# Performance work log

Hardware: AMD Instinct MI355X
Metric: run time of the kernel (lower is better)

## Reference

```python
import jax, jax.numpy as jnp
import numpy as np

EMB = 768
HEADS = 8

def setup_inputs() -> dict:
    key = jax.random.key(0)
    ks = jax.random.split(key, 9)
    B, N, E = 16, 1024, EMB
    s = 1.0 / np.sqrt(E)
    x = jax.random.normal(ks[0], (B, N, E), dtype=jnp.float32)
    Wq = jax.random.normal(ks[1], (E, E), dtype=jnp.float32) * s
    bq = jnp.zeros((E,), dtype=jnp.float32)
    Wk = jax.random.normal(ks[2], (E, E), dtype=jnp.float32) * s
    bk = jnp.zeros((E,), dtype=jnp.float32)
    Wv = jax.random.normal(ks[3], (E, E), dtype=jnp.float32) * s
    bv = jnp.zeros((E,), dtype=jnp.float32)
    Wo = jax.random.normal(ks[4], (E, E), dtype=jnp.float32) * s
    bo = jnp.zeros((E,), dtype=jnp.float32)
    return {"x": x, "Wq": Wq, "bq": bq, "Wk": Wk, "bk": bk, "Wv": Wv, "bv": bv, "Wo": Wo, "bo": bo}

def reference(x, Wq, bq, Wk, bk, Wv, bv, Wo, bo):
    B, N, E = x.shape
    H = HEADS
    D = E // H
    # separate Q/K/V linears, split heads: b n (h d) -> b h n d
    q = (x @ Wq + bq).reshape(B, N, H, D).transpose(0, 2, 1, 3)
    k = (x @ Wk + bk).reshape(B, N, H, D).transpose(0, 2, 1, 3)
    v = (x @ Wv + bv).reshape(B, N, H, D).transpose(0, 2, 1, 3)
    energy = jnp.einsum('bhqd,bhkd->bhqk', q, k)
    # NON-STANDARD: softmax first, then divide by sqrt(emb_size)
    scaling = jnp.float32(E) ** 0.5
    attn = jax.nn.softmax(energy, axis=-1) / scaling
    out = jnp.einsum('bhqk,bhkd->bhqd', attn, v)
    out = out.transpose(0, 2, 1, 3).reshape(B, N, E)  # b h n d -> b n (h d)
    return out @ Wo + bo
```

## Files before the change

kernel.cpp:

```cpp
#include <hip/hip_runtime.h>


typedef _Float16 half8 __attribute__((ext_vector_type(8)));
typedef __fp16 fp16x2 __attribute__((ext_vector_type(2)));
typedef float f32x4 __attribute__((ext_vector_type(4)));

__device__ __forceinline__ void gload_lds16(const void* g, void* l) {
  __builtin_amdgcn_global_load_lds((const __attribute__((address_space(1))) void*)g,
                                   (__attribute__((address_space(3))) void*)l, 16, 0, 0);
}


__global__ __launch_bounds__(256) void conv_x_kernel(const float* __restrict__ x,
                                                     _Float16* __restrict__ xh) {
  long i = ((long)blockIdx.x * 256 + threadIdx.x) * 8;
  float4 a = *(const float4*)(x + i);
  float4 b = *(const float4*)(x + i + 4);
  half8 o;
  o[0] = (_Float16)a.x; o[1] = (_Float16)a.y; o[2] = (_Float16)a.z; o[3] = (_Float16)a.w;
  o[4] = (_Float16)b.x; o[5] = (_Float16)b.y; o[6] = (_Float16)b.z; o[7] = (_Float16)b.w;
  *(half8*)(xh + i) = o;
}

__global__ __launch_bounds__(256) void transpose_cvt_kernel(
    const float* __restrict__ W0, const float* __restrict__ W1,
    const float* __restrict__ W2, const float* __restrict__ W3,
    _Float16* __restrict__ WT) {
  __shared__ float tile[32][33];
  int z = blockIdx.z;
  const float* W = (z == 0) ? W0 : (z == 1) ? W1 : (z == 2) ? W2 : W3;
  int k0 = blockIdx.y * 32, n0 = blockIdx.x * 32;
  int tx = threadIdx.x, ty = threadIdx.y;
#pragma unroll
  for (int j = ty; j < 32; j += 8)
    tile[j][tx] = W[(size_t)(k0 + j) * 768 + n0 + tx];
  __syncthreads();
  _Float16* dst = WT + (size_t)z * 768 * 768;
#pragma unroll
  for (int j = ty; j < 32; j += 8)
    dst[(size_t)(n0 + j) * 768 + k0 + tx] = (_Float16)tile[tx][j];
}

__global__ __launch_bounds__(256) void conv_bias_kernel(const float* __restrict__ bq,
                                                        const float* __restrict__ bk,
                                                        const float* __restrict__ bv,
                                                        float* __restrict__ bias) {
  int i = blockIdx.x * 256 + threadIdx.x;
  if (i >= 2304) return;
  bias[i] = (i < 768) ? bq[i] : (i < 1536) ? bk[i - 768] : bv[i - 1536];
}


template <int OUT_F16>
__global__ __launch_bounds__(512, 2) void gemm256_kernel(
    const _Float16* __restrict__ A, const _Float16* __restrict__ Bt,
    const float* __restrict__ bias, void* __restrict__ C,
    int M, int N, int K, int ldc) {
  __shared__ _Float16 As[2][256 * 64];
  __shared__ _Float16 Bs[2][256 * 64];
  int nbx = N >> 8;
  int nwg = gridDim.x, wg = blockIdx.x;
  int cpx = nwg >> 3;
  int swz = (wg & 7) * cpx + (wg >> 3);
  int bx = swz % nbx, by = swz / nbx;
  int m0 = by * 256, n0 = bx * 256;
  int t = threadIdx.x, l = t & 63, w = t >> 6;
  int lg = l >> 4, lr = l & 15;
  int wr = w >> 2, wc = w & 3;
  f32x4 acc[8][4] = {};

  int srow[4], ssc[4];
#pragma unroll
  for (int j = 0; j < 4; ++j) {
    int slot = j * 512 + t;
    srow[j] = slot >> 3;
    ssc[j] = ((slot & 7) ^ (srow[j] & 7)) * 8;
  }

  auto stage = [&](int kt, int bi) {
    int k0 = kt * 64;
#pragma unroll
    for (int j = 0; j < 4; ++j)
      gload_lds16(A + (size_t)(m0 + srow[j]) * K + k0 + ssc[j], &As[bi][(j * 512 + t) * 8]);
#pragma unroll
    for (int j = 0; j < 4; ++j)
      gload_lds16(Bt + (size_t)(n0 + srow[j]) * K + k0 + ssc[j], &Bs[bi][(j * 512 + t) * 8]);
  };

  auto compute = [&](int bi) {
#pragma unroll
    for (int kk = 0; kk < 2; ++kk) {
      half8 bf[4];
#pragma unroll
      for (int nf = 0; nf < 4; ++nf) {
        int row = wc * 64 + nf * 16 + lr;
        bf[nf] = *(const half8*)&Bs[bi][row * 64 + ((kk * 4 + lg) ^ (row & 7)) * 8];
      }
#pragma unroll
      for (int mf = 0; mf < 8; ++mf) {
        int row = wr * 128 + mf * 16 + lr;
        half8 af = *(const half8*)&As[bi][row * 64 + ((kk * 4 + lg) ^ (row & 7)) * 8];
#pragma unroll
        for (int nf = 0; nf < 4; ++nf)
          acc[mf][nf] = __builtin_amdgcn_mfma_f32_16x16x32_f16(af, bf[nf], acc[mf][nf], 0, 0, 0);
      }
    }
  };

  int nkt = K >> 6;
  stage(0, 0);
  for (int kt = 0; kt < nkt; ++kt) {
    int bi = kt & 1;
    if (kt + 1 < nkt) {
      stage(kt + 1, bi ^ 1);
      asm volatile("s_waitcnt vmcnt(8)" ::: "memory");
    } else {
      asm volatile("s_waitcnt vmcnt(0)" ::: "memory");
    }
    __builtin_amdgcn_sched_barrier(0);
    __builtin_amdgcn_s_barrier();
    __builtin_amdgcn_sched_barrier(0);
    compute(bi);
    __builtin_amdgcn_sched_barrier(0);
    __builtin_amdgcn_s_barrier();
  }

#pragma unroll
  for (int mf = 0; mf < 8; ++mf)
#pragma unroll
    for (int nf = 0; nf < 4; ++nf) {
      int col = n0 + wc * 64 + nf * 16 + lr;
      float bb = bias[col];
#pragma unroll
      for (int i = 0; i < 4; ++i) {
        int row = m0 + wr * 128 + mf * 16 + lg * 4 + i;
        float v = acc[mf][nf][i] + bb;
        if (OUT_F16)
          ((_Float16*)C)[(size_t)row * ldc + col] = (_Float16)v;
        else
          ((float*)C)[(size_t)row * ldc + col] = v;
      }
    }
}


__global__ __launch_bounds__(512) void attn_kernel(const _Float16* __restrict__ QKV,
                                                   _Float16* __restrict__ Oh) {
  int hw = blockIdx.x;
  int lin = (hw & 7) * 128 + (hw >> 3);
  int bh = lin >> 3, qt = lin & 7;
  int b = bh >> 3, h = bh & 7;
  int t = threadIdx.x, w = t >> 6, l = t & 63;
  int lg = l >> 4, lr = l & 15;

  __shared__ _Float16 Ks[2][64 * 128];
  __shared__ _Float16 Vts[2][96 * 64];
  __shared__ _Float16 Ps[8][16 * 64];

  const _Float16* Qb = QKV + (size_t)b * 1024 * 2304 + h * 96;
  const _Float16* Kb = Qb + 768;
  const _Float16* Vb = Qb + 1536;

  half8 qf[3];
  {
    int qrow = qt * 128 + w * 16 + lr;
    const _Float16 s = (_Float16)1.4426950408889634f;
#pragma unroll
    for (int c = 0; c < 3; ++c) {
      qf[c] = *(const half8*)&Qb[(size_t)qrow * 2304 + c * 32 + lg * 8];
#pragma unroll
      for (int e = 0; e < 8; ++e) qf[c][e] = qf[c][e] * s;
    }
  }

  int ksrc[2], kdst[2];
#pragma unroll
  for (int j = 0; j < 2; ++j) {
    int slot = j * 512 + t;
    int kv = slot >> 4, seg = slot & 15;
    ksrc[j] = kv * 2304 + (seg ^ (kv & 7)) * 8;
    kdst[j] = slot * 8;
  }
  bool vact = t < 384;
  int kvp = t / 12, m = t % 12;
  int vsrc = 2 * kvp * 2304 + m * 8;
  int vdst[8];
#pragma unroll
  for (int e = 0; e < 8; ++e) {
    int d = m * 8 + e;
    int sw = ((d & 7) ^ ((d >> 3) & 7)) << 3;
    vdst[e] = d * 64 + ((2 * kvp) ^ sw);
  }
  int swq = (lr & 7) << 3;
  int poff[4];
#pragma unroll
  for (int tt = 0; tt < 4; ++tt) poff[tt] = lr * 64 + ((tt * 16 + lg * 4) ^ swq);

  auto stage = [&](int kv0, int bi) {
    size_t goff = (size_t)kv0 * 2304;
#pragma unroll
    for (int j = 0; j < 2; ++j)
      gload_lds16(Kb + goff + ksrc[j], &Ks[bi][kdst[j]]);
    if (vact) {
      const _Float16* vp = Vb + goff + vsrc;
      half8 v0 = *(const half8*)vp;
      half8 v1 = *(const half8*)(vp + 2304);
#pragma unroll
      for (int e = 0; e < 8; ++e) {
        union { _Float16 h2[2]; unsigned u32; } pk;
        pk.h2[0] = v0[e]; pk.h2[1] = v1[e];
        *(unsigned*)&Vts[bi][vdst[e]] = pk.u32;
      }
    }
  };

  float m_run = -3.0e38f, l_run = 0.f;
  f32x4 o_acc[6] = {};

  stage(0, 0);

  for (int tile = 0; tile < 16; ++tile) {
    int bi = tile & 1;
    __syncthreads();
    if (tile + 1 < 16) stage((tile + 1) * 64, bi ^ 1);

    f32x4 s_acc[4];
#pragma unroll
    for (int tt = 0; tt < 4; ++tt) {
      s_acc[tt] = f32x4{0.f, 0.f, 0.f, 0.f};
      int kvr = tt * 16 + lr;
#pragma unroll
      for (int c = 0; c < 3; ++c) {
        half8 kf = *(const half8*)&Ks[bi][kvr * 128 + ((c * 4 + lg) ^ (kvr & 7)) * 8];
        s_acc[tt] = __builtin_amdgcn_mfma_f32_16x16x32_f16(kf, qf[c], s_acc[tt], 0, 0, 0);
      }
    }

    float tmax = -3.0e38f;
#pragma unroll
    for (int tt = 0; tt < 4; ++tt)
#pragma unroll
      for (int i = 0; i < 4; ++i) tmax = fmaxf(tmax, s_acc[tt][i]);
    tmax = fmaxf(tmax, __shfl_xor(tmax, 16, 64));
    tmax = fmaxf(tmax, __shfl_xor(tmax, 32, 64));

    if (!__all(tmax <= m_run + 11.5f)) {
      float m_new = fmaxf(m_run, tmax);
      float scale = __builtin_exp2f(m_run - m_new);
      float sc0 = __shfl(scale, lg * 4 + 0, 64);
      float sc1 = __shfl(scale, lg * 4 + 1, 64);
      float sc2 = __shfl(scale, lg * 4 + 2, 64);
      float sc3 = __shfl(scale, lg * 4 + 3, 64);
#pragma unroll
      for (int cc = 0; cc < 6; ++cc) {
        o_acc[cc][0] *= sc0; o_acc[cc][1] *= sc1;
        o_acc[cc][2] *= sc2; o_acc[cc][3] *= sc3;
      }
      l_run *= scale;
      m_run = m_new;
    }

    float rs = 0.f;
#pragma unroll
    for (int tt = 0; tt < 4; ++tt) {
      float p0 = __builtin_exp2f(s_acc[tt][0] - m_run);
      float p1 = __builtin_exp2f(s_acc[tt][1] - m_run);
      float p2 = __builtin_exp2f(s_acc[tt][2] - m_run);
      float p3 = __builtin_exp2f(s_acc[tt][3] - m_run);
      rs += (p0 + p1) + (p2 + p3);
      union { fp16x2 h2[2]; unsigned long long u64; } pk;
      pk.h2[0] = __builtin_amdgcn_cvt_pkrtz(p0, p1);
      pk.h2[1] = __builtin_amdgcn_cvt_pkrtz(p2, p3);
      *(unsigned long long*)&Ps[w][poff[tt]] = pk.u64;
    }
    rs += __shfl_xor(rs, 16, 64);
    rs += __shfl_xor(rs, 32, 64);
    l_run += rs;

#pragma unroll
    for (int kc = 0; kc < 2; ++kc) {
      half8 pf = *(const half8*)&Ps[w][lr * 64 + ((kc * 32 + lg * 8) ^ swq)];
#pragma unroll
      for (int cc = 0; cc < 6; ++cc) {
        int d = cc * 16 + lr;
        int sw = ((d & 7) ^ ((d >> 3) & 7)) << 3;
        half8 vf = *(const half8*)&Vts[bi][d * 64 + ((kc * 32 + lg * 8) ^ sw)];
        o_acc[cc] = __builtin_amdgcn_mfma_f32_16x16x32_f16(pf, vf, o_acc[cc], 0, 0, 0);
      }
    }
  }

  float inv = 1.0f / (l_run * 27.712812921102035f);
  float iv0 = __shfl(inv, lg * 4 + 0, 64);
  float iv1 = __shfl(inv, lg * 4 + 1, 64);
  float iv2 = __shfl(inv, lg * 4 + 2, 64);
  float iv3 = __shfl(inv, lg * 4 + 3, 64);
  size_t rbase = (size_t)(b * 1024 + qt * 128 + w * 16) * 768 + h * 96;
#pragma unroll
  for (int cc = 0; cc < 6; ++cc) {
    int col = cc * 16 + lr;
    Oh[rbase + (size_t)(lg * 4 + 0) * 768 + col] = (_Float16)(o_acc[cc][0] * iv0);
    Oh[rbase + (size_t)(lg * 4 + 1) * 768 + col] = (_Float16)(o_acc[cc][1] * iv1);
    Oh[rbase + (size_t)(lg * 4 + 2) * 768 + col] = (_Float16)(o_acc[cc][2] * iv2);
    Oh[rbase + (size_t)(lg * 4 + 3) * 768 + col] = (_Float16)(o_acc[cc][3] * iv3);
  }
}


extern "C" void kernel_launch(void* const* d_in, const int* in_sizes, int n_in,
                              void* d_out, int out_size, void* d_ws, size_t ws_size,
                              hipStream_t stream) {
  const float* x  = (const float*)d_in[0];
  const float* Wq = (const float*)d_in[1];
  const float* bq = (const float*)d_in[2];
  const float* Wk = (const float*)d_in[3];
  const float* bk = (const float*)d_in[4];
  const float* Wv = (const float*)d_in[5];
  const float* bv = (const float*)d_in[6];
  const float* Wo = (const float*)d_in[7];
  const float* bo = (const float*)d_in[8];
  float* out = (float*)d_out;

  char* ws = (char*)d_ws;
  _Float16* WT   = (_Float16*)(ws);
  float*    bias = (float*)(ws + 4718592);
  _Float16* xh   = (_Float16*)(ws + 4751360);
  _Float16* QKV  = (_Float16*)(ws + 29917184);
  _Float16* Oh   = (_Float16*)(ws + 105414656);

  conv_x_kernel<<<6144, 256, 0, stream>>>(x, xh);
  transpose_cvt_kernel<<<dim3(24, 24, 4), dim3(32, 8), 0, stream>>>(Wq, Wk, Wv, Wo, WT);
  conv_bias_kernel<<<9, 256, 0, stream>>>(bq, bk, bv, bias);

  gemm256_kernel<1><<<576, 512, 0, stream>>>(xh, WT, bias, QKV, 16384, 2304, 768, 2304);

  attn_kernel<<<1024, 512, 0, stream>>>(QKV, Oh);

  gemm256_kernel<0><<<192, 512, 0, stream>>>(Oh, WT + (size_t)2304 * 768, bo, out,
                                             16384, 768, 768, 768);
}
```

Measured before the change: 232.5 us.

## Rewrite attention with 32x32x16 MFMA, register-resident P, 4-wave blocks

The attention kernel moves from 16x16x32 to 32x32x16 MFMA tiles, with each wave owning 32 query rows. K is staged into LDS already in MFMA fragment order. The P matrix no longer round-trips through LDS; lanes swap halves with a cross-lane shuffle to form the A operand for the PV MFMA. Blocks drop to 256 threads with a two-blocks-per-CU launch bound, which cuts LDS traffic and P staging at the cost of more registers per lane and extra shuffles.

Result: slower. 420.6 us (+80.9%).

```diff
diff --git a/kernel.cpp b/kernel.cpp
--- a/kernel.cpp
+++ b/kernel.cpp
@@ -4,6 +4,7 @@
 typedef _Float16 half8 __attribute__((ext_vector_type(8)));
 typedef __fp16 fp16x2 __attribute__((ext_vector_type(2)));
 typedef float f32x4 __attribute__((ext_vector_type(4)));
+typedef float f32x16 __attribute__((ext_vector_type(16)));
 
 __device__ __forceinline__ void gload_lds16(const void* g, void* l) {
   __builtin_amdgcn_global_load_lds((const __attribute__((address_space(1))) void*)g,
@@ -144,78 +145,81 @@
 }
 
 
-__global__ __launch_bounds__(512) void attn_kernel(const _Float16* __restrict__ QKV,
-                                                   _Float16* __restrict__ Oh) {
+__global__ __launch_bounds__(256, 2) void attn_kernel(const _Float16* __restrict__ QKV,
+                                                      _Float16* __restrict__ Oh) {
   int hw = blockIdx.x;
   int lin = (hw & 7) * 128 + (hw >> 3);
   int bh = lin >> 3, qt = lin & 7;
   int b = bh >> 3, h = bh & 7;
   int t = threadIdx.x, w = t >> 6, l = t & 63;
-  int lg = l >> 4, lr = l & 15;
-
-  __shared__ _Float16 Ks[2][64 * 128];
-  __shared__ _Float16 Vts[2][96 * 64];
-  __shared__ _Float16 Ps[8][16 * 64];
+  int lr = l & 31, hi = l >> 5;
+
+  __shared__ __align__(16) char KF[2][12288];
+  __shared__ __align__(16) _Float16 VF[2][96 * 64];
 
   const _Float16* Qb = QKV + (size_t)b * 1024 * 2304 + h * 96;
   const _Float16* Kb = Qb + 768;
   const _Float16* Vb = Qb + 1536;
 
-  half8 qf[3];
+  half8 qf[6];
   {
-    int qrow = qt * 128 + w * 16 + lr;
+    int qrow = qt * 128 + w * 32 + lr;
     const _Float16 s = (_Float16)1.4426950408889634f;
 #pragma unroll
-    for (int c = 0; c < 3; ++c) {
-      qf[c] = *(const half8*)&Qb[(size_t)qrow * 2304 + c * 32 + lg * 8];
+    for (int c = 0; c < 6; ++c) {
+      qf[c] = *(const half8*)&Qb[(size_t)qrow * 2304 + c * 16 + hi * 8];
 #pragma unroll
       for (int e = 0; e < 8; ++e) qf[c][e] = qf[c][e] * s;
     }
   }
 
-  int ksrc[2], kdst[2];
+  int ks_src[3], ks_dst[3];
+#pragma unroll
+  for (int j = 0; j < 3; ++j) {
+    int s = j * 256 + t;
+    int f = s >> 6, lane = s & 63;
+    int sb = f / 6, c = f - sb * 6;
+    ks_src[j] = (sb * 32 + (lane & 31)) * 2304 + c * 16 + ((lane >> 5) & 1) * 8;
+    ks_dst[j] = s * 16;
+  }
+  bool vact[2];
+  int v_src[2], v_dst[2][8];
 #pragma unroll
   for (int j = 0; j < 2; ++j) {
-    int slot = j * 512 + t;
-    int kv = slot >> 4, seg = slot & 15;
-    ksrc[j] = kv * 2304 + (seg ^ (kv & 7)) * 8;
-    kdst[j] = slot * 8;
-  }
-  bool vact = t < 384;
-  int kvp = t / 12, m = t % 12;
-  int vsrc = 2 * kvp * 2304 + m * 8;
-  int vdst[8];
-#pragma unroll
-  for (int e = 0; e < 8; ++e) {
-    int d = m * 8 + e;
-    int sw = ((d & 7) ^ ((d >> 3) & 7)) << 3;
-    vdst[e] = d * 64 + ((2 * kvp) ^ sw);
-  }
-  int swq = (lr & 7) << 3;
-  int poff[4];
-#pragma unroll
-  for (int tt = 0; tt < 4; ++tt) poff[tt] = lr * 64 + ((tt * 16 + lg * 4) ^ swq);
+    int u = j * 256 + t;
+    vact[j] = u < 384;
+    int kvp = u / 12, mm = u % 12;
+    v_src[j] = 2 * kvp * 2304 + mm * 8;
+#pragma unroll
+    for (int e = 0; e < 8; ++e) {
+      int d = mm * 8 + e;
+      int sw = ((d & 7) ^ ((d >> 3) & 7)) << 3;
+      v_dst[j][e] = d * 64 + ((2 * kvp) ^ sw);
+    }
+  }
 
   auto stage = [&](int kv0, int bi) {
     size_t goff = (size_t)kv0 * 2304;
 #pragma unroll
+    for (int j = 0; j < 3; ++j)
+      gload_lds16(Kb + goff + ks_src[j], &KF[bi][ks_dst[j]]);
+#pragma unroll
     for (int j = 0; j < 2; ++j)
-      gload_lds16(Kb + goff + ksrc[j], &Ks[bi][kdst[j]]);
-    if (vact) {
-      const _Float16* vp = Vb + goff + vsrc;
-      half8 v0 = *(const half8*)vp;
-      half8 v1 = *(const half8*)(vp + 2304);
-#pragma unroll
-      for (int e = 0; e < 8; ++e) {
-        union { _Float16 h2[2]; unsigned u32; } pk;
-        pk.h2[0] = v0[e]; pk.h2[1] = v1[e];
-        *(unsigned*)&Vts[bi][vdst[e]] = pk.u32;
-      }
-    }
+      if (vact[j]) {
+        const _Float16* vp = Vb + goff + v_src[j];
+        half8 v0 = *(const half8*)vp;
+        half8 v1 = *(const half8*)(vp + 2304);
+#pragma unroll
+        for (int e = 0; e < 8; ++e) {
+          union { _Float16 h2[2]; unsigned u32; } pk;
+          pk.h2[0] = v0[e]; pk.h2[1] = v1[e];
+          *(unsigned*)&VF[bi][v_dst[j][e]] = pk.u32;
+        }
+      }
   };
 
   float m_run = -3.0e38f, l_run = 0.f;
-  f32x4 o_acc[6] = {};
+  f32x16 oa[3] = {};
 
   stage(0, 0);
 
@@ -224,85 +228,89 @@
     __syncthreads();
     if (tile + 1 < 16) stage((tile + 1) * 64, bi ^ 1);
 
-    f32x4 s_acc[4];
-#pragma unroll
-    for (int tt = 0; tt < 4; ++tt) {
-      s_acc[tt] = f32x4{0.f, 0.f, 0.f, 0.f};
-      int kvr = tt * 16 + lr;
-#pragma unroll
-      for (int c = 0; c < 3; ++c) {
-        half8 kf = *(const half8*)&Ks[bi][kvr * 128 + ((c * 4 + lg) ^ (kvr & 7)) * 8];
-        s_acc[tt] = __builtin_amdgcn_mfma_f32_16x16x32_f16(kf, qf[c], s_acc[tt], 0, 0, 0);
-      }
-    }
+    f32x16 sA[2] = {};
+#pragma unroll
+    for (int sb = 0; sb < 2; ++sb)
+#pragma unroll
+      for (int c = 0; c < 6; ++c) {
+        half8 kf = *(const half8*)(KF[bi] + (sb * 6 + c) * 1024 + l * 16);
+        sA[sb] = __builtin_amdgcn_mfma_f32_32x32x16_f16(kf, qf[c], sA[sb], 0, 0, 0);
+      }
 
     float tmax = -3.0e38f;
 #pragma unroll
-    for (int tt = 0; tt < 4; ++tt)
-#pragma unroll
-      for (int i = 0; i < 4; ++i) tmax = fmaxf(tmax, s_acc[tt][i]);
-    tmax = fmaxf(tmax, __shfl_xor(tmax, 16, 64));
+    for (int sb = 0; sb < 2; ++sb)
+#pragma unroll
+      for (int r = 0; r < 16; ++r) tmax = fmaxf(tmax, sA[sb][r]);
     tmax = fmaxf(tmax, __shfl_xor(tmax, 32, 64));
 
     if (!__all(tmax <= m_run + 11.5f)) {
       float m_new = fmaxf(m_run, tmax);
       float scale = __builtin_exp2f(m_run - m_new);
-      float sc0 = __shfl(scale, lg * 4 + 0, 64);
-      float sc1 = __shfl(scale, lg * 4 + 1, 64);
-      float sc2 = __shfl(scale, lg * 4 + 2, 64);
-      float sc3 = __shfl(scale, lg * 4 + 3, 64);
-#pragma unroll
-      for (int cc = 0; cc < 6; ++cc) {
-        o_acc[cc][0] *= sc0; o_acc[cc][1] *= sc1;
-        o_acc[cc][2] *= sc2; o_acc[cc][3] *= sc3;
+#pragma unroll
+      for (int r = 0; r < 16; ++r) {
+        float sr = __shfl(scale, (r & 3) + 8 * (r >> 2) + 4 * hi, 64);
+        oa[0][r] *= sr; oa[1][r] *= sr; oa[2][r] *= sr;
       }
       l_run *= scale;
       m_run = m_new;
     }
 
+    unsigned keep[8], send[8];
     float rs = 0.f;
 #pragma unroll
-    for (int tt = 0; tt < 4; ++tt) {
-      float p0 = __builtin_exp2f(s_acc[tt][0] - m_run);
-      float p1 = __builtin_exp2f(s_acc[tt][1] - m_run);
-      float p2 = __builtin_exp2f(s_acc[tt][2] - m_run);
-      float p3 = __builtin_exp2f(s_acc[tt][3] - m_run);
-      rs += (p0 + p1) + (p2 + p3);
-      union { fp16x2 h2[2]; unsigned long long u64; } pk;
-      pk.h2[0] = __builtin_amdgcn_cvt_pkrtz(p0, p1);
-      pk.h2[1] = __builtin_amdgcn_cvt_pkrtz(p2, p3);
-      *(unsigned long long*)&Ps[w][poff[tt]] = pk.u64;
-    }
-    rs += __shfl_xor(rs, 16, 64);
+    for (int sb = 0; sb < 2; ++sb)
+#pragma unroll
+      for (int kb = 0; kb < 2; ++kb)
+#pragma unroll
+        for (int m = 0; m < 2; ++m) {
+          int rk = 2 * m + 8 * kb + 4 * hi;
+          int rq = 2 * m + 8 * kb + 4 * (1 - hi);
+          float k0 = __builtin_exp2f(sA[sb][rk] - m_run);
+          float k1 = __builtin_exp2f(sA[sb][rk + 1] - m_run);
+          float q0 = __builtin_exp2f(sA[sb][rq] - m_run);
+          float q1 = __builtin_exp2f(sA[sb][rq + 1] - m_run);
+          rs += (k0 + k1) + (q0 + q1);
+          union { fp16x2 h2; unsigned u; } a, bb;
+          a.h2 = __builtin_amdgcn_cvt_pkrtz(k0, k1);
+          bb.h2 = __builtin_amdgcn_cvt_pkrtz(q0, q1);
+          keep[sb * 4 + kb * 2 + m] = a.u;
+          send[sb * 4 + kb * 2 + m] = bb.u;
+        }
     rs += __shfl_xor(rs, 32, 64);
     l_run += rs;
 
-#pragma unroll
-    for (int kc = 0; kc < 2; ++kc) {
-      half8 pf = *(const half8*)&Ps[w][lr * 64 + ((kc * 32 + lg * 8) ^ swq)];
-#pragma unroll
-      for (int cc = 0; cc < 6; ++cc) {
-        int d = cc * 16 + lr;
+    unsigned recv[8];
+#pragma unroll
+    for (int i = 0; i < 8; ++i) recv[i] = __shfl_xor(send[i], 32, 64);
+
+#pragma unroll
+    for (int kstep = 0; kstep < 4; ++kstep) {
+      int base = (kstep >> 1) * 4 + (kstep & 1) * 2;
+      union { unsigned u[4]; half8 h8; } pa;
+      pa.u[0] = hi ? recv[base + 0] : keep[base + 0];
+      pa.u[1] = hi ? recv[base + 1] : keep[base + 1];
+      pa.u[2] = hi ? keep[base + 0] : recv[base + 0];
+      pa.u[3] = hi ? keep[base + 1] : recv[base + 1];
+#pragma unroll
+      for (int dt = 0; dt < 3; ++dt) {
+        int d = dt * 32 + lr;
         int sw = ((d & 7) ^ ((d >> 3) & 7)) << 3;
-        half8 vf = *(const half8*)&Vts[bi][d * 64 + ((kc * 32 + lg * 8) ^ sw)];
-        o_acc[cc] = __builtin_amdgcn_mfma_f32_16x16x32_f16(pf, vf, o_acc[cc], 0, 0, 0);
+        half8 vf = *(const half8*)&VF[bi][d * 64 + ((kstep * 16 + hi * 8) ^ sw)];
+        oa[dt] = __builtin_amdgcn_mfma_f32_32x32x16_f16(pa.h8, vf, oa[dt], 0, 0, 0);
       }
     }
   }
 
   float inv = 1.0f / (l_run * 27.712812921102035f);
-  float iv0 = __shfl(inv, lg * 4 + 0, 64);
-  float iv1 = __shfl(inv, lg * 4 + 1, 64);
-  float iv2 = __shfl(inv, lg * 4 + 2, 64);
-  float iv3 = __shfl(inv, lg * 4 + 3, 64);
-  size_t rbase = (size_t)(b * 1024 + qt * 128 + w * 16) * 768 + h * 96;
-#pragma unroll
-  for (int cc = 0; cc < 6; ++cc) {
-    int col = cc * 16 + lr;
-    Oh[rbase + (size_t)(lg * 4 + 0) * 768 + col] = (_Float16)(o_acc[cc][0] * iv0);
-    Oh[rbase + (size_t)(lg * 4 + 1) * 768 + col] = (_Float16)(o_acc[cc][1] * iv1);
-    Oh[rbase + (size_t)(lg * 4 + 2) * 768 + col] = (_Float16)(o_acc[cc][2] * iv2);
-    Oh[rbase + (size_t)(lg * 4 + 3) * 768 + col] = (_Float16)(o_acc[cc][3] * iv3);
+  size_t rbase = (size_t)(b * 1024 + qt * 128 + w * 32) * 768 + h * 96;
+#pragma unroll
+  for (int r = 0; r < 16; ++r) {
+    int q = (r & 3) + 8 * (r >> 2) + 4 * hi;
+    float ivr = __shfl(inv, q, 64);
+#pragma unroll
+    for (int dt = 0; dt < 3; ++dt)
+      Oh[rbase + (size_t)q * 768 + dt * 32 + lr] = (_Float16)(oa[dt][r] * ivr);
   }
 }
 
@@ -334,7 +342,7 @@
 
   gemm256_kernel<1><<<576, 512, 0, stream>>>(xh, WT, bias, QKV, 16384, 2304, 768, 2304);
 
-  attn_kernel<<<1024, 512, 0, stream>>>(QKV, Oh);
+  attn_kernel<<<1024, 256, 0, stream>>>(QKV, Oh);
 
   gemm256_kernel<0><<<192, 512, 0, stream>>>(Oh, WT + (size_t)2304 * 768, bo, out,
                                              16384, 768, 768, 768);
```
